# Optimization experiments

Hardware: AMD Instinct MI355X
Metric: run time of the kernel (lower is better)

The kernel has to match this reference:

```python
import jax, jax.numpy as jnp
import numpy as np

EMBED_DIM = 512
HEADS = 8
ATTN_DIM = EMBED_DIM // HEADS
PF_DIM = 2048
B, L = 4, 2048
LN_EPS = 1e-5


def _linear(x, W, b):
    # nn.Linear: x @ W.T + b, W is [out, in]
    return jnp.einsum('bld,od->blo', x, W) + b


def _layer_norm(x, g, b):
    mu = jnp.mean(x, axis=-1, keepdims=True)
    var = jnp.mean(jnp.square(x - mu), axis=-1, keepdims=True)
    return (x - mu) * jax.lax.rsqrt(var + LN_EPS) * g + b


def _qkv(src, Wq, bq, Wk, bk, Wv, bv):
    def split(t):
        Bb, Ll, _ = t.shape
        return t.reshape(Bb, Ll, HEADS, ATTN_DIM).transpose(0, 2, 1, 3)  # [B,H,L,Dh]
    return (split(_linear(src, Wq, bq)),
            split(_linear(src, Wk, bk)),
            split(_linear(src, Wv, bv)))


def _attention(inp, Q, K1, K2, V1, V2, Wo, bo, ln_g, ln_b, W1, b1, W2, b2):
    # non-softmax linear attention: (Q K1^T) V1 + (Q K2^T) V2
    attn = (jnp.einsum('bhqk,bhkd->bhqd', jnp.einsum('bhqd,bhkd->bhqk', Q, K1), V1)
            + jnp.einsum('bhqk,bhkd->bhqd', jnp.einsum('bhqd,bhkd->bhqk', Q, K2), V2))
    Bb = Q.shape[0]
    attn = attn.transpose(0, 2, 1, 3).reshape(Bb, -1, HEADS * ATTN_DIM)  # [B,L,D]
    x = _linear(attn, Wo, bo)
    x = _layer_norm(inp + x, ln_g, ln_b)          # dropout p=0 (eval)
    ff = _linear(jax.nn.relu(_linear(x, W1, b1)), W2, b2)
    x = _layer_norm(x + ff, ln_g, ln_b)
    return x


def setup_inputs() -> dict:
    key = jax.random.key(0)
    ks = jax.random.split(key, 16)
    s = 0.02
    return {
        'question': jax.random.normal(ks[0], (B, L, EMBED_DIM), jnp.float32),
        'query': jax.random.normal(ks[1], (B, L, EMBED_DIM), jnp.float32),
        'Wq': jax.random.normal(ks[2], (EMBED_DIM, EMBED_DIM), jnp.float32) * s,
        'bq': jnp.zeros((EMBED_DIM,), jnp.float32),
        'Wk': jax.random.normal(ks[3], (EMBED_DIM, EMBED_DIM), jnp.float32) * s,
        'bk': jnp.zeros((EMBED_DIM,), jnp.float32),
        'Wv': jax.random.normal(ks[4], (EMBED_DIM, EMBED_DIM), jnp.float32) * s,
        'bv': jnp.zeros((EMBED_DIM,), jnp.float32),
        'Wo': jax.random.normal(ks[5], (EMBED_DIM, EMBED_DIM), jnp.float32) * s,
        'bo': jnp.zeros((EMBED_DIM,), jnp.float32),
        'ln_g': jnp.ones((EMBED_DIM,), jnp.float32),
        'ln_b': jnp.zeros((EMBED_DIM,), jnp.float32),
        'W1': jax.random.normal(ks[6], (PF_DIM, EMBED_DIM), jnp.float32) * s,
        'b1': jnp.zeros((PF_DIM,), jnp.float32),
        'W2': jax.random.normal(ks[7], (EMBED_DIM, PF_DIM), jnp.float32) * s,
        'b2': jnp.zeros((EMBED_DIM,), jnp.float32),
    }


def reference(question, query, Wq, bq, Wk, bk, Wv, bv, Wo, bo, ln_g, ln_b, W1, b1, W2, b2):
    Q1, K1, V1 = _qkv(question, Wq, bq, Wk, bk, Wv, bv)
    Q2, K2, V2 = _qkv(query, Wq, bq, Wk, bk, Wv, bv)
    question_attn = _attention(question, Q1, K1, K2, V1, V2, Wo, bo, ln_g, ln_b, W1, b1, W2, b2)
    query_attn = _attention(query, Q2, K2, K1, V2, V1, Wo, bo, ln_g, ln_b, W1, b1, W2, b2)
    return jnp.concatenate([question_attn, query_attn], axis=-1)
```

## Files before the change

### kernel.cpp

```cpp
#include <hip/hip_runtime.h>
#include <stdint.h>


#define Bq 4
#define Lq 2048
#define Dq 512
#define PFq 2048
#define Mrows 16384
#define MiBu 1048576ull
#define NSLICE 16

typedef __attribute__((ext_vector_type(8))) short frag_ab;
typedef __attribute__((ext_vector_type(4))) float frag_cd;
typedef __attribute__((ext_vector_type(8))) unsigned short ushort8v;

__device__ __forceinline__ unsigned short f2b(float f) {
    union { float f; uint32_t u; } x; x.f = f;
    uint32_t r = x.u + 0x7fffu + ((x.u >> 16) & 1u);
    return (unsigned short)(r >> 16);
}
__device__ __forceinline__ float b2f(unsigned short u) {
    union { uint32_t u; float f; } x; x.u = ((uint32_t)u) << 16;
    return x.f;
}

#define GLD16(g, l)                                                              \
    __builtin_amdgcn_global_load_lds(                                            \
        (const __attribute__((address_space(1))) void*)(const void*)(g),         \
        (__attribute__((address_space(3))) void*)(void*)(l), 16, 0, 0)

#define STG(BUFOFS, REGOFS, GB, ROWOFS, TILE, KS)                                \
    { GLD16((GB) + (size_t)(ROWOFS) * (KS) + (size_t)(TILE) * 64,                \
            Sh + (BUFOFS) + (REGOFS) + ld);                                      \
      GLD16((GB) + ((size_t)(ROWOFS) + 64) * (KS) + (size_t)(TILE) * 64,         \
            Sh + (BUFOFS) + (REGOFS) + ld + 4096); }

#define VMW(N) asm volatile("s_waitcnt vmcnt(" #N ")" ::: "memory")

#define PHASE(CB, M0, LOADB, STAGE_STMT, WAIT_STMT)                              \
    {                                                                            \
        frag_ab a00 = *(const frag_ab*)&Sh[(CB) + (wm + (M0)*16 + lr) * 64 + xo0];      \
        frag_ab a01 = *(const frag_ab*)&Sh[(CB) + (wm + (M0)*16 + lr) * 64 + xo1];      \
        frag_ab a10 = *(const frag_ab*)&Sh[(CB) + (wm + (M0)*16 + 16 + lr) * 64 + xo0]; \
        frag_ab a11 = *(const frag_ab*)&Sh[(CB) + (wm + (M0)*16 + 16 + lr) * 64 + xo1]; \
        if (LOADB) {                                                             \
            _Pragma("unroll")                                                    \
            for (int j = 0; j < 4; ++j) {                                        \
                bf[j][0] = *(const frag_ab*)&Sh[(CB) + 16384 + (wn + j*16 + lr)*64 + xo0]; \
                bf[j][1] = *(const frag_ab*)&Sh[(CB) + 16384 + (wn + j*16 + lr)*64 + xo1]; \
            }                                                                    \
        }                                                                        \
        STAGE_STMT;                                                              \
        WAIT_STMT;                                                               \
        __builtin_amdgcn_sched_barrier(0);                                       \
        __builtin_amdgcn_s_barrier();                                            \
        asm volatile("s_waitcnt lgkmcnt(0)" ::: "memory");                       \
        __builtin_amdgcn_sched_barrier(0);                                       \
        __builtin_amdgcn_s_setprio(1);                                           \
        _Pragma("unroll")                                                        \
        for (int j = 0; j < 4; ++j) {                                            \
            acc[(M0)][j]   = __builtin_amdgcn_mfma_f32_16x16x32_bf16(a00, bf[j][0], acc[(M0)][j], 0,0,0);   \
            acc[(M0)][j]   = __builtin_amdgcn_mfma_f32_16x16x32_bf16(a01, bf[j][1], acc[(M0)][j], 0,0,0);   \
            acc[(M0)+1][j] = __builtin_amdgcn_mfma_f32_16x16x32_bf16(a10, bf[j][0], acc[(M0)+1][j], 0,0,0); \
            acc[(M0)+1][j] = __builtin_amdgcn_mfma_f32_16x16x32_bf16(a11, bf[j][1], acc[(M0)+1][j], 0,0,0); \
        }                                                                        \
        __builtin_amdgcn_s_setprio(0);                                           \
        __builtin_amdgcn_sched_barrier(0);                                       \
        __builtin_amdgcn_s_barrier();                                            \
        __builtin_amdgcn_sched_barrier(0);                                       \
    }

__global__ __launch_bounds__(512, 2) void gemm_256(
    const unsigned short* __restrict__ A, const unsigned short* __restrict__ Wt,
    const float* __restrict__ bias, unsigned short* __restrict__ outB,
    int M, int N, int relu)
{
    __shared__ __align__(16) unsigned short Sh[65536];
    const int tid = threadIdx.x;
    const int lane = tid & 63;
    const int w = tid >> 6;
    const int wm = (w >> 2) * 128;
    const int wn = (w & 3) * 64;
    const int lr = lane & 15;
    const int quad = lane >> 4;
    const int xo0 = ((quad ^ (lr & 7)) << 3);
    const int xo1 = (((4 | quad) ^ (lr & 7)) << 3);

    const int b0 = blockIdx.x;
    const int xcd = b0 & 7, slot = b0 >> 3;
    const int mloc = (M >> 8) >> 3;
    const size_t bm = (size_t)(xcd * mloc + slot % mloc) * 256;
    const size_t bn = (size_t)(slot / mloc) * 256;

    const int ar = tid >> 3;
    const int sw = ((tid & 7) ^ (ar & 7)) << 3;
    const unsigned short* Ag = A  + (bm + ar) * (size_t)512 + sw;
    const unsigned short* Bg = Wt + (bn + ar) * (size_t)512 + sw;
    const int ld = tid * 8;

    frag_cd acc[8][4] = {};
    frag_ab bf[4][2];

    STG(0,     16384, Bg, 0,   0, 512);
    STG(0,     24576, Bg, 128, 0, 512);
    STG(0,     0,     Ag, 0,   0, 512);
    STG(0,     8192,  Ag, 128, 0, 512);
    STG(32768, 16384, Bg, 0,   1, 512);
    STG(32768, 24576, Bg, 128, 1, 512);
    VMW(4);
    __builtin_amdgcn_sched_barrier(0);
    __builtin_amdgcn_s_barrier();
    __builtin_amdgcn_sched_barrier(0);

    for (int I = 0; I < 3; ++I) {
        const int tb = 2 * I + 1, tc = 2 * I + 2, td = 2 * I + 3;
        PHASE(0,     0, 1, STG(32768, 0,     Ag, 0,   tb, 512), (void)0);
        PHASE(0,     2, 0, STG(32768, 8192,  Ag, 128, tb, 512), (void)0);
        PHASE(0,     4, 0, STG(0,     16384, Bg, 0,   tc, 512), (void)0);
        PHASE(0,     6, 0, STG(0,     24576, Bg, 128, tc, 512), VMW(4));
        PHASE(32768, 0, 1, STG(0,     0,     Ag, 0,   tc, 512), (void)0);
        PHASE(32768, 2, 0, STG(0,     8192,  Ag, 128, tc, 512), (void)0);
        PHASE(32768, 4, 0, STG(32768, 16384, Bg, 0,   td, 512), (void)0);
        PHASE(32768, 6, 0, STG(32768, 24576, Bg, 128, td, 512), VMW(4));
    }
    PHASE(0,     0, 1, STG(32768, 0,    Ag, 0,   7, 512), (void)0);
    PHASE(0,     2, 0, STG(32768, 8192, Ag, 128, 7, 512), (void)0);
    PHASE(0,     4, 0, (void)0, (void)0);
    PHASE(0,     6, 0, (void)0, VMW(0));
    PHASE(32768, 0, 1, (void)0, (void)0);
    PHASE(32768, 2, 0, (void)0, (void)0);
    PHASE(32768, 4, 0, (void)0, (void)0);
    PHASE(32768, 6, 0, (void)0, (void)0);

    float bv[4];
#pragma unroll
    for (int j = 0; j < 4; ++j) bv[j] = bias[(int)bn + wn + j * 16 + lr];
    unsigned short* Cs = Sh + w * 8192;
#pragma unroll
    for (int m = 0; m < 8; ++m)
#pragma unroll
        for (int j = 0; j < 4; ++j)
#pragma unroll
            for (int r = 0; r < 4; ++r) {
                float v = acc[m][j][r] + bv[j];
                if (relu) v = fmaxf(v, 0.f);
                Cs[(m * 16 + quad * 4 + r) * 64 + j * 16 + lr] = f2b(v);
            }
    const int rl = lane >> 3, c8 = (lane & 7) * 8;
#pragma unroll
    for (int k = 0; k < 16; ++k) {
        const int row = rl + k * 8;
        ushort8v val = *(const ushort8v*)&Cs[row * 64 + c8];
        *(ushort8v*)(outB + (size_t)(bm + wm + row) * N + bn + wn + c8) = val;
    }
}

__global__ __launch_bounds__(512, 2) void gemm_n128(
    const unsigned short* __restrict__ A, const unsigned short* __restrict__ Wt,
    const float* __restrict__ bias,
    const float* __restrict__ resA, const float* __restrict__ resB,
    unsigned short* __restrict__ outB, int N, int K, int mode, int perb)
{
    __shared__ __align__(16) unsigned short Sh[49152];
    const int tid = threadIdx.x;
    const int lane = tid & 63;
    const int w = tid >> 6;
    const int wm = (w >> 1) * 64;
    const int wn = (w & 1) * 64;
    const int lr = lane & 15;
    const int quad = lane >> 4;
    const int xo0 = ((quad ^ (lr & 7)) << 3);
    const int xo1 = (((4 | quad) ^ (lr & 7)) << 3);

    const int b0 = blockIdx.x;
    const int xcd = b0 & 7, slot = b0 >> 3;
    const size_t bm = (size_t)(xcd * 8 + (slot & 7)) * 256;
    const size_t bn = (size_t)(slot >> 3) * 128;

    if (perb) {
        const int bsel = ((int)(bm >> 11)) & 3;
        Wt += (size_t)bsel << 18;
        bias += bsel << 9;
    }

    const int ar = tid >> 3;
    const int sw = ((tid & 7) ^ (ar & 7)) << 3;
    const unsigned short* Ag = A  + (bm + ar) * (size_t)K + sw;
    const unsigned short* Bg = Wt + (bn + ar) * (size_t)K + sw;
    const int ld = tid * 8;

    frag_cd acc[4][4] = {};
    frag_ab bf[4][2];

    STG(0,     16384, Bg, 0,   0, K);
    STG(0,     0,     Ag, 0,   0, K);
    STG(0,     8192,  Ag, 128, 0, K);
    STG(24576, 16384, Bg, 0,   1, K);
    VMW(2);
    __builtin_amdgcn_sched_barrier(0);
    __builtin_amdgcn_s_barrier();
    __builtin_amdgcn_sched_barrier(0);

    const int nIter = K >> 7;
    for (int I = 0; I < nIter - 1; ++I) {
        const int tb = 2 * I + 1, tc = 2 * I + 2, td = 2 * I + 3;
        PHASE(0,     0, 1, { STG(24576, 0, Ag, 0, tb, K); STG(24576, 8192, Ag, 128, tb, K); }, (void)0);
        PHASE(0,     2, 0, STG(0, 16384, Bg, 0, tc, K), VMW(2));
        PHASE(24576, 0, 1, { STG(0, 0, Ag, 0, tc, K); STG(0, 8192, Ag, 128, tc, K); }, (void)0);
        PHASE(24576, 2, 0, STG(24576, 16384, Bg, 0, td, K), VMW(2));
    }
    {
        const int tb = (K >> 6) - 1;
        PHASE(0,     0, 1, { STG(24576, 0, Ag, 0, tb, K); STG(24576, 8192, Ag, 128, tb, K); }, (void)0);
        PHASE(0,     2, 0, (void)0, VMW(0));
        PHASE(24576, 0, 1, (void)0, (void)0);
        PHASE(24576, 2, 0, (void)0, (void)0);
    }

    float bv[4];
#pragma unroll
    for (int j = 0; j < 4; ++j) bv[j] = bias[(int)bn + wn + j * 16 + lr];
    unsigned short* Cs = Sh + w * 4096;
#pragma unroll
    for (int m = 0; m < 4; ++m)
#pragma unroll
        for (int j = 0; j < 4; ++j)
#pragma unroll
            for (int r = 0; r < 4; ++r)
                Cs[(m * 16 + quad * 4 + r) * 64 + j * 16 + lr] = f2b(acc[m][j][r] + bv[j]);
    const int rl = lane >> 3, c8 = (lane & 7) * 8;
#pragma unroll
    for (int k = 0; k < 8; ++k) {
        const int row = rl + k * 8;
        const int grow = (int)bm + wm + row;
        const size_t idx = (size_t)grow * N + bn + wn + c8;
        ushort8v val = *(const ushort8v*)&Cs[row * 64 + c8];
        if (mode == 0) {
            *(ushort8v*)(outB + idx) = val;
            continue;
        }
        float vv[8];
#pragma unroll
        for (int t2 = 0; t2 < 8; ++t2) vv[t2] = b2f(val[t2]);
        if (mode == 1) {
            const float* rp = (grow < 8192) ? resA + idx : resB + idx - (size_t)8192 * N;
            float4 ra = *(const float4*)(rp);
            float4 rb = *(const float4*)(rp + 4);
            vv[0] += ra.x; vv[1] += ra.y; vv[2] += ra.z; vv[3] += ra.w;
            vv[4] += rb.x; vv[5] += rb.y; vv[6] += rb.z; vv[7] += rb.w;
        } else {
            ushort8v old = *(const ushort8v*)(outB + idx);
#pragma unroll
            for (int t2 = 0; t2 < 8; ++t2) vv[t2] += b2f(old[t2]);
        }
        ushort8v o;
#pragma unroll
        for (int t2 = 0; t2 < 8; ++t2) o[t2] = f2b(vv[t2]);
        *(ushort8v*)(outB + idx) = o;
    }
}

__global__ __launch_bounds__(256) void gemm_fuse(
    const unsigned short* __restrict__ Wob, const unsigned short* __restrict__ UT,
    unsigned short* __restrict__ Wfin)
{
    __shared__ __align__(16) unsigned short Sh[2 * 128 * 64];
    unsigned short* At = Sh;
    unsigned short* Bt = Sh + 128 * 64;
    const int tid = threadIdx.x;
    const int lane = tid & 63;
    const int w = tid >> 6;
    const int wm = (w >> 1) * 64, wn = (w & 1) * 64;
    const int lr = lane & 15;
    const int quad = lane >> 4;
    const int bb = blockIdx.z;
    const size_t bm = (size_t)blockIdx.x * 128, bn = (size_t)blockIdx.y * 128;

    frag_cd acc[4][4] = {};
    const int ar = tid >> 3;
    const int acs = (((tid & 7) ^ (ar & 7)) << 3);
    const unsigned short* Ag = Wob + (bm + ar) * 512 + acs;
    const unsigned short* Bg = UT + ((size_t)bb << 18) + (bn + ar) * 512 + acs;
    unsigned short* Asd = At + w * 512;
    unsigned short* Bsd = Bt + w * 512;

    for (int k0 = 0; k0 < 512; k0 += 64) {
        __syncthreads();
#pragma unroll
        for (int i = 0; i < 4; ++i) {
            GLD16(Ag + (size_t)(32 * i) * 512 + k0, Asd + i * 2048);
            GLD16(Bg + (size_t)(32 * i) * 512 + k0, Bsd + i * 2048);
        }
        __syncthreads();
#pragma unroll
        for (int kk = 0; kk < 2; ++kk) {
            frag_ab a[4], b[4];
#pragma unroll
            for (int i = 0; i < 4; ++i)
                a[i] = *(const frag_ab*)&At[(wm + i * 16 + lr) * 64 +
                                            ((((kk << 2) | quad) ^ (lr & 7)) << 3)];
#pragma unroll
            for (int j = 0; j < 4; ++j)
                b[j] = *(const frag_ab*)&Bt[(wn + j * 16 + lr) * 64 +
                                            ((((kk << 2) | quad) ^ (lr & 7)) << 3)];
#pragma unroll
            for (int i = 0; i < 4; ++i)
#pragma unroll
                for (int j = 0; j < 4; ++j)
                    acc[i][j] = __builtin_amdgcn_mfma_f32_16x16x32_bf16(a[i], b[j], acc[i][j], 0, 0, 0);
        }
    }
    __syncthreads();
    unsigned short* Cs = Sh + w * 4096;
#pragma unroll
    for (int j = 0; j < 4; ++j)
#pragma unroll
        for (int i = 0; i < 4; ++i)
#pragma unroll
            for (int r = 0; r < 4; ++r)
                Cs[(i * 16 + quad * 4 + r) * 64 + j * 16 + lr] = f2b(acc[i][j][r]);
    const int rl = lane >> 3, c8 = (lane & 7) * 8;
#pragma unroll
    for (int k = 0; k < 8; ++k) {
        const int row = rl + k * 8;
        ushort8v val = *(const ushort8v*)&Cs[row * 64 + c8];
        *(ushort8v*)(Wfin + ((size_t)bb << 18) + (bm + wm + row) * 512 + bn + wn + c8) = val;
    }
}

__global__ __launch_bounds__(256) void convert_all(
    const float* __restrict__ Wq, const float* __restrict__ Wk,
    const float* __restrict__ Wv, const float* __restrict__ Wo,
    const float* __restrict__ W1, const float* __restrict__ W2,
    const float* __restrict__ question, const float* __restrict__ query,
    const float* __restrict__ bqp, const float* __restrict__ bkp,
    const float* __restrict__ bvp, const float* __restrict__ bo,
    unsigned short* __restrict__ Wqkvb, unsigned short* __restrict__ Wob,
    unsigned short* __restrict__ W1b, unsigned short* __restrict__ W2b,
    unsigned short* __restrict__ Xb, float* __restrict__ bqkv,
    float* __restrict__ biasO)
{
    const int b = blockIdx.x;
    const float* src; unsigned short* dst; size_t off;
    if (b < 256)        { src = Wq; dst = Wqkvb;          off = (size_t)b * 1024; }
    else if (b < 512)   { src = Wk; dst = Wqkvb + 262144; off = (size_t)(b - 256) * 1024; }
    else if (b < 768)   { src = Wv; dst = Wqkvb + 524288; off = (size_t)(b - 512) * 1024; }
    else if (b < 1024)  { src = Wo; dst = Wob;            off = (size_t)(b - 768) * 1024; }
    else if (b < 2048)  { src = W1; dst = W1b;            off = (size_t)(b - 1024) * 1024; }
    else if (b < 3072)  { src = W2; dst = W2b;            off = (size_t)(b - 2048) * 1024; }
    else if (b < 7168)  { src = question; dst = Xb;       off = (size_t)(b - 3072) * 1024; }
    else if (b < 11264) { src = query; dst = Xb + 4194304; off = (size_t)(b - 7168) * 1024; }
    else if (b < 11270) {
        const int n = (b - 11264) * 256 + threadIdx.x;
        bqkv[n] = (n < 512) ? bqp[n] : (n < 1024) ? bkp[n - 512] : bvp[n - 1024];
        return;
    } else {
        const int n = (b - 11270) * 256 + threadIdx.x;
        biasO[n] = bo[n & 511];
        return;
    }
    const size_t idx = off + threadIdx.x * 4;
    float4 v = *(const float4*)(src + idx);
    ushort4 o;
    o.x = f2b(v.x); o.y = f2b(v.y); o.z = f2b(v.z); o.w = f2b(v.w);
    *(ushort4*)(dst + idx) = o;
}

__global__ __launch_bounds__(256) void s_kernel(
    const unsigned short* __restrict__ QKV, float* __restrict__ Spart)
{
    const int bh = blockIdx.x;
    const int sl = blockIdx.y;
    const int b = bh >> 3, h = bh & 7;
    const int pass = sl >> 3;
    const int l0 = (sl & 7) * 256;
    __shared__ float Ks[64][64];
    __shared__ float Vs[64][64];
    const int tid = threadIdx.x;
    const int tx = tid & 15, ty = tid >> 4;
    const int srow = tid >> 3;
    const int scol = (tid & 7) * 8;
    const size_t rowbase = (size_t)pass * 8192 + (size_t)b * Lq + l0;

    float acc[4][4] = {};

    for (int t0 = 0; t0 < 256; t0 += 64) {
        const unsigned short* kp0 = QKV + (rowbase + t0 + srow) * 1024 + h * 64 + scol;
        const unsigned short* kp1 = kp0 + (size_t)32 * 1024;
        ushort8v k0 = *(const ushort8v*)kp0;
        ushort8v v0 = *(const ushort8v*)(kp0 + 512);
        ushort8v k1 = *(const ushort8v*)kp1;
        ushort8v v1 = *(const ushort8v*)(kp1 + 512);
        __syncthreads();
#pragma unroll
        for (int e = 0; e < 8; ++e) {
            Ks[srow][scol + e]      = b2f(k0[e]);
            Vs[srow][scol + e]      = b2f(v0[e]);
            Ks[srow + 32][scol + e] = b2f(k1[e]);
            Vs[srow + 32][scol + e] = b2f(v1[e]);
        }
        __syncthreads();
#pragma unroll 4
        for (int rr = 0; rr < 64; ++rr) {
            const float4 kf = *(const float4*)&Ks[rr][ty * 4];
            const float4 vf = *(const float4*)&Vs[rr][tx * 4];
            acc[0][0] = fmaf(kf.x, vf.x, acc[0][0]);
            acc[0][1] = fmaf(kf.x, vf.y, acc[0][1]);
            acc[0][2] = fmaf(kf.x, vf.z, acc[0][2]);
            acc[0][3] = fmaf(kf.x, vf.w, acc[0][3]);
            acc[1][0] = fmaf(kf.y, vf.x, acc[1][0]);
            acc[1][1] = fmaf(kf.y, vf.y, acc[1][1]);
            acc[1][2] = fmaf(kf.y, vf.z, acc[1][2]);
            acc[1][3] = fmaf(kf.y, vf.w, acc[1][3]);
            acc[2][0] = fmaf(kf.z, vf.x, acc[2][0]);
            acc[2][1] = fmaf(kf.z, vf.y, acc[2][1]);
            acc[2][2] = fmaf(kf.z, vf.z, acc[2][2]);
            acc[2][3] = fmaf(kf.z, vf.w, acc[2][3]);
            acc[3][0] = fmaf(kf.w, vf.x, acc[3][0]);
            acc[3][1] = fmaf(kf.w, vf.y, acc[3][1]);
            acc[3][2] = fmaf(kf.w, vf.z, acc[3][2]);
            acc[3][3] = fmaf(kf.w, vf.w, acc[3][3]);
        }
    }

    float* Sp = Spart + ((size_t)bh * NSLICE + sl) * 4096;
#pragma unroll
    for (int i = 0; i < 4; ++i) {
        float4 o = make_float4(acc[i][0], acc[i][1], acc[i][2], acc[i][3]);
        *(float4*)(Sp + (ty * 4 + i) * 64 + tx * 4) = o;
    }
}

__global__ __launch_bounds__(256) void s_reduce(
    const float* __restrict__ Spart, float* __restrict__ Sred)
{
    const int bh = blockIdx.x, uo = blockIdx.y;
    const float* Sp = Spart + (size_t)bh * (NSLICE * 4096);
    float* Dp = Sred + (size_t)bh * 4096;
    const int t = threadIdx.x;
#pragma unroll
    for (int u = 0; u < 4; ++u) {
        const int d = (uo * 4 + u) * 256 + t;
        float v = 0.f;
#pragma unroll
        for (int s = 0; s < NSLICE; ++s) v += Sp[(size_t)s * 4096 + d];
        Dp[d] = v;
    }
}

__global__ __launch_bounds__(512) void u_kernel(
    const float* __restrict__ Sred, const unsigned short* __restrict__ Wqb,
    const unsigned short* __restrict__ Wob, const float* __restrict__ bq,
    unsigned short* __restrict__ UT, float* __restrict__ biasO)
{
    const int bh = blockIdx.x, jh = blockIdx.y;
    const int b = bh >> 3, h = bh & 7;
    __shared__ float Sf[4096];
    __shared__ float rsh[32];
    const int t = threadIdx.x;
#pragma unroll
    for (int e = 0; e < 8; ++e)
        Sf[e * 512 + t] = Sred[(size_t)bh * 4096 + e * 512 + t];
    __syncthreads();

    const int j0 = jh * 32;
    float T[32] = {};
    for (int k = 0; k < 64; ++k) {
        const float wq = b2f(Wqb[(h * 64 + k) * 512 + t]);
#pragma unroll
        for (int j = 0; j < 32; ++j)
            T[j] = fmaf(wq, Sf[k * 64 + j0 + j], T[j]);
    }
    unsigned short* up = UT + ((size_t)(b * 512 + t)) * 512 + h * 64 + j0;
#pragma unroll
    for (int g = 0; g < 4; ++g) {
        ushort8v o;
#pragma unroll
        for (int e = 0; e < 8; ++e) o[e] = f2b(T[g * 8 + e]);
        *(ushort8v*)(up + g * 8) = o;
    }

    if (t < 32) {
        float r = 0.f;
        for (int k = 0; k < 64; ++k) r += bq[h * 64 + k] * Sf[k * 64 + j0 + t];
        rsh[t] = r;
    }
    __syncthreads();
    float c = 0.f;
#pragma unroll
    for (int j = 0; j < 32; ++j)
        c += rsh[j] * b2f(Wob[(size_t)t * 512 + h * 64 + j0 + j]);
    atomicAdd(&biasO[b * 512 + t], c);
}

__global__ __launch_bounds__(256) void ln_b16_inplace(
    unsigned short* __restrict__ Y, const float* __restrict__ g,
    const float* __restrict__ bta)
{
    __shared__ float part[8];
    const int row = blockIdx.x;
    const int t = threadIdx.x;
    const int w = t >> 6;
    unsigned short* yr = Y + (size_t)row * Dq;
    const float v0 = b2f(yr[t]), v1 = b2f(yr[t + 256]);
    float s = v0 + v1;
#pragma unroll
    for (int off = 32; off; off >>= 1) s += __shfl_xor(s, off, 64);
    if ((t & 63) == 0) part[w] = s;
    __syncthreads();
    const float mean = (part[0] + part[1] + part[2] + part[3]) * (1.f / Dq);
    const float d0 = v0 - mean, d1 = v1 - mean;
    float q = d0 * d0 + d1 * d1;
#pragma unroll
    for (int off = 32; off; off >>= 1) q += __shfl_xor(q, off, 64);
    if ((t & 63) == 0) part[4 + w] = q;
    __syncthreads();
    const float rstd = rsqrtf((part[4] + part[5] + part[6] + part[7]) * (1.f / Dq) + 1e-5f);
    yr[t] = f2b(d0 * rstd * g[t] + bta[t]);
    yr[t + 256] = f2b(d1 * rstd * g[t + 256] + bta[t + 256]);
}

__global__ __launch_bounds__(256) void ln_b16_out(
    const unsigned short* __restrict__ Y, const float* __restrict__ g,
    const float* __restrict__ bta, float* __restrict__ out)
{
    __shared__ float part[8];
    const int row = blockIdx.x;
    const int t = threadIdx.x;
    const int w = t >> 6;
    const unsigned short* yr = Y + (size_t)row * Dq;
    const float v0 = b2f(yr[t]), v1 = b2f(yr[t + 256]);
    float s = v0 + v1;
#pragma unroll
    for (int off = 32; off; off >>= 1) s += __shfl_xor(s, off, 64);
    if ((t & 63) == 0) part[w] = s;
    __syncthreads();
    const float mean = (part[0] + part[1] + part[2] + part[3]) * (1.f / Dq);
    const float d0 = v0 - mean, d1 = v1 - mean;
    float q = d0 * d0 + d1 * d1;
#pragma unroll
    for (int off = 32; off; off >>= 1) q += __shfl_xor(q, off, 64);
    if ((t & 63) == 0) part[4 + w] = q;
    __syncthreads();
    const float rstd = rsqrtf((part[4] + part[5] + part[6] + part[7]) * (1.f / Dq) + 1e-5f);
    const int half = row >> 13, br = row & 8191;
    float* orow = out + (size_t)br * 1024 + half * 512;
    orow[t] = d0 * rstd * g[t] + bta[t];
    orow[t + 256] = d1 * rstd * g[t + 256] + bta[t + 256];
}

extern "C" void kernel_launch(void* const* d_in, const int* in_sizes, int n_in,
                              void* d_out, int out_size, void* d_ws, size_t ws_size,
                              hipStream_t stream)
{
    const float* question = (const float*)d_in[0];
    const float* query    = (const float*)d_in[1];
    const float* Wq = (const float*)d_in[2];  const float* bqp = (const float*)d_in[3];
    const float* Wk = (const float*)d_in[4];  const float* bkp = (const float*)d_in[5];
    const float* Wv = (const float*)d_in[6];  const float* bvp = (const float*)d_in[7];
    const float* Wo = (const float*)d_in[8];  const float* bo  = (const float*)d_in[9];
    const float* ln_g = (const float*)d_in[10]; const float* ln_b = (const float*)d_in[11];
    const float* W1 = (const float*)d_in[12]; const float* b1 = (const float*)d_in[13];
    const float* W2 = (const float*)d_in[14]; const float* b2 = (const float*)d_in[15];
    float* out = (float*)d_out;
    char* ws = (char*)d_ws;

    unsigned short* QKVb = (unsigned short*)(ws);
    unsigned short* UT   = (unsigned short*)(ws + 32 * MiBu);
    unsigned short* Wfin = (unsigned short*)(ws + 34 * MiBu);
    float* Sred          = (float*)(ws + 36 * MiBu);
    float* Spart         = (float*)(ws + 40 * MiBu);
    unsigned short* hb   = (unsigned short*)(ws);
    unsigned short* xbuf = (unsigned short*)(ws + 64 * MiBu);
    unsigned short* Xb   = (unsigned short*)d_out;
    char* wp = ws + 80 * MiBu;
    unsigned short* Wqkvb = (unsigned short*)wp;  wp += 1536 * 512 * 2;
    unsigned short* Wob   = (unsigned short*)wp;  wp += 512 * 512 * 2;
    unsigned short* W1b   = (unsigned short*)wp;  wp += 2048 * 512 * 2;
    unsigned short* W2b   = (unsigned short*)wp;  wp += 512 * 2048 * 2;
    float* biasO          = (float*)wp;           wp += 4 * 512 * 4;
    float* bqkv           = (float*)wp;

    dim3 blk(256);

    convert_all<<<11278, blk, 0, stream>>>(Wq, Wk, Wv, Wo, W1, W2, question, query,
                                           bqp, bkp, bvp, bo,
                                           Wqkvb, Wob, W1b, W2b, Xb, bqkv, biasO);

    gemm_n128<<<dim3(512), dim3(512), 0, stream>>>(Xb, Wqkvb + 262144, bqkv + 512,
                                                   nullptr, nullptr, QKVb,
                                                   1024, 512, 0, 0);

    s_kernel<<<dim3(32, NSLICE), blk, 0, stream>>>(QKVb, Spart);
    s_reduce<<<dim3(32, 4), blk, 0, stream>>>(Spart, Sred);
    u_kernel<<<dim3(32, 2), dim3(512), 0, stream>>>(Sred, Wqkvb, Wob, bqkv, UT, biasO);
    gemm_fuse<<<dim3(4, 4, 4), blk, 0, stream>>>(Wob, UT, Wfin);

    gemm_n128<<<dim3(256), dim3(512), 0, stream>>>(Xb, Wfin, biasO,
                                                   question, query, xbuf,
                                                   512, 512, 1, 1);

    ln_b16_inplace<<<Mrows, blk, 0, stream>>>(xbuf, ln_g, ln_b);

    gemm_256<<<dim3(512), dim3(512), 0, stream>>>(xbuf, W1b, b1, hb,
                                                  Mrows, PFq, 1);

    gemm_n128<<<dim3(256), dim3(512), 0, stream>>>(hb, W2b, b2,
                                                   nullptr, nullptr, xbuf,
                                                   512, 2048, 2, 0);

    ln_b16_out<<<Mrows, blk, 0, stream>>>(xbuf, ln_g, ln_b, out);
}
```

Baseline: 311.8 us.

## Fold S reduction into u_kernel, use gemm_256 for K/V projection, bf16 residual

The separate s_reduce kernel is removed, and u_kernel now sums the NSLICE partial S matrices itself while filling shared memory. This saves a launch and a global round trip. The K/V projection GEMM now uses the 256-wide gemm_256 kernel instead of gemm_n128. The Wo residual add reads the bf16 copy of the inputs (Xb) through a new mode instead of the fp32 question/query tensors, which halves residual read bytes but rounds the residual to bf16.

```diff
diff --git a/kernel.cpp b/kernel.cpp
--- a/kernel.cpp
+++ b/kernel.cpp
@@ -159,6 +159,7 @@
     const unsigned short* __restrict__ A, const unsigned short* __restrict__ Wt,
     const float* __restrict__ bias,
     const float* __restrict__ resA, const float* __restrict__ resB,
+    const unsigned short* __restrict__ res16,
     unsigned short* __restrict__ outB, int N, int K, int mode, int perb)
 {
     __shared__ __align__(16) unsigned short Sh[49152];
@@ -249,7 +250,8 @@
             vv[0] += ra.x; vv[1] += ra.y; vv[2] += ra.z; vv[3] += ra.w;
             vv[4] += rb.x; vv[5] += rb.y; vv[6] += rb.z; vv[7] += rb.w;
         } else {
-            ushort8v old = *(const ushort8v*)(outB + idx);
+            const unsigned short* rp16 = (mode == 2) ? (outB + idx) : (res16 + idx);
+            ushort8v old = *(const ushort8v*)rp16;
 #pragma unroll
             for (int t2 = 0; t2 < 8; ++t2) vv[t2] += b2f(old[t2]);
         }
@@ -431,25 +433,8 @@
     }
 }
 
-__global__ __launch_bounds__(256) void s_reduce(
-    const float* __restrict__ Spart, float* __restrict__ Sred)
-{
-    const int bh = blockIdx.x, uo = blockIdx.y;
-    const float* Sp = Spart + (size_t)bh * (NSLICE * 4096);
-    float* Dp = Sred + (size_t)bh * 4096;
-    const int t = threadIdx.x;
-#pragma unroll
-    for (int u = 0; u < 4; ++u) {
-        const int d = (uo * 4 + u) * 256 + t;
-        float v = 0.f;
-#pragma unroll
-        for (int s = 0; s < NSLICE; ++s) v += Sp[(size_t)s * 4096 + d];
-        Dp[d] = v;
-    }
-}
-
 __global__ __launch_bounds__(512) void u_kernel(
-    const float* __restrict__ Sred, const unsigned short* __restrict__ Wqb,
+    const float* __restrict__ Spart, const unsigned short* __restrict__ Wqb,
     const unsigned short* __restrict__ Wob, const float* __restrict__ bq,
     unsigned short* __restrict__ UT, float* __restrict__ biasO)
 {
@@ -458,9 +443,15 @@
     __shared__ float Sf[4096];
     __shared__ float rsh[32];
     const int t = threadIdx.x;
-#pragma unroll
-    for (int e = 0; e < 8; ++e)
-        Sf[e * 512 + t] = Sred[(size_t)bh * 4096 + e * 512 + t];
+    const float* Sp = Spart + (size_t)bh * (NSLICE * 4096);
+#pragma unroll
+    for (int e = 0; e < 8; ++e) {
+        const int d = e * 512 + t;
+        float v = 0.f;
+#pragma unroll
+        for (int s = 0; s < NSLICE; ++s) v += Sp[(size_t)s * 4096 + d];
+        Sf[d] = v;
+    }
     __syncthreads();
 
     const int j0 = jh * 32;
@@ -568,7 +559,6 @@
     unsigned short* QKVb = (unsigned short*)(ws);
     unsigned short* UT   = (unsigned short*)(ws + 32 * MiBu);
     unsigned short* Wfin = (unsigned short*)(ws + 34 * MiBu);
-    float* Sred          = (float*)(ws + 36 * MiBu);
     float* Spart         = (float*)(ws + 40 * MiBu);
     unsigned short* hb   = (unsigned short*)(ws);
     unsigned short* xbuf = (unsigned short*)(ws + 64 * MiBu);
@@ -587,18 +577,16 @@
                                            bqp, bkp, bvp, bo,
                                            Wqkvb, Wob, W1b, W2b, Xb, bqkv, biasO);
 
-    gemm_n128<<<dim3(512), dim3(512), 0, stream>>>(Xb, Wqkvb + 262144, bqkv + 512,
-                                                   nullptr, nullptr, QKVb,
-                                                   1024, 512, 0, 0);
+    gemm_256<<<dim3(256), dim3(512), 0, stream>>>(Xb, Wqkvb + 262144, bqkv + 512,
+                                                  QKVb, Mrows, 1024, 0);
 
     s_kernel<<<dim3(32, NSLICE), blk, 0, stream>>>(QKVb, Spart);
-    s_reduce<<<dim3(32, 4), blk, 0, stream>>>(Spart, Sred);
-    u_kernel<<<dim3(32, 2), dim3(512), 0, stream>>>(Sred, Wqkvb, Wob, bqkv, UT, biasO);
+    u_kernel<<<dim3(32, 2), dim3(512), 0, stream>>>(Spart, Wqkvb, Wob, bqkv, UT, biasO);
     gemm_fuse<<<dim3(4, 4, 4), blk, 0, stream>>>(Wob, UT, Wfin);
 
     gemm_n128<<<dim3(256), dim3(512), 0, stream>>>(Xb, Wfin, biasO,
-                                                   question, query, xbuf,
-                                                   512, 512, 1, 1);
+                                                   nullptr, nullptr, Xb, xbuf,
+                                                   512, 512, 3, 1);
 
     ln_b16_inplace<<<Mrows, blk, 0, stream>>>(xbuf, ln_g, ln_b);
 
@@ -606,7 +594,7 @@
                                                   Mrows, PFq, 1);
 
     gemm_n128<<<dim3(256), dim3(512), 0, stream>>>(hb, W2b, b2,
-                                                   nullptr, nullptr, xbuf,
+                                                   nullptr, nullptr, nullptr, xbuf,
                                                    512, 2048, 2, 0);
 
     ln_b16_out<<<Mrows, blk, 0, stream>>>(xbuf, ln_g, ln_b, out);
```

New measurement: 310.2 us. Within noise of the previous version (-0.5%).
